# Kernel tuning notes

Hardware: AMD Instinct MI355X
Metric: run time of the kernel (lower is better)

The kernel has to match this reference:

```python
import jax, jax.numpy as jnp
import numpy as np
from jax import lax


def _lin_weights(in_size, out_size):
    # torch F.interpolate(mode='bilinear', align_corners=False) source indices
    scale = in_size / out_size
    src = (jnp.arange(out_size, dtype=jnp.float32) + 0.5) * scale - 0.5
    src = jnp.maximum(src, 0.0)
    i0 = jnp.minimum(jnp.floor(src).astype(jnp.int32), in_size - 1)
    i1 = jnp.minimum(i0 + 1, in_size - 1)
    w = src - i0.astype(jnp.float32)
    return i0, i1, w


def bilinear_resize(x, out_h, out_w):
    # x: (..., H, W) -> (..., out_h, out_w), separable bilinear
    H, W = x.shape[-2], x.shape[-1]
    i0, i1, wh = _lin_weights(H, out_h)
    j0, j1, ww = _lin_weights(W, out_w)
    x = x[..., i0, :] * (1.0 - wh)[:, None] + x[..., i1, :] * wh[:, None]
    x = x[..., :, j0] * (1.0 - ww) + x[..., :, j1] * ww
    return x


def setup_inputs() -> dict:
    key = jax.random.key(0)
    ks = jax.random.split(key, 16)
    b, H, W = 16, 56, 56
    n = H * W
    dim, heads, dh, agent_num = 512, 8, 64, 49
    ID = heads * dh  # inner_dim == dim
    s = 0.02
    return {
        'x': jax.random.normal(ks[0], (b, n, dim), jnp.float32),
        'H': H, 'W': W,
        'q_w': s * jax.random.normal(ks[1], (dim, ID), jnp.float32),
        'q_b': s * jax.random.normal(ks[2], (ID,), jnp.float32),
        'kv_w': s * jax.random.normal(ks[3], (dim, 2 * ID), jnp.float32),
        'kv_b': s * jax.random.normal(ks[4], (2 * ID,), jnp.float32),
        'proj_w': s * jax.random.normal(ks[5], (ID, dim), jnp.float32),
        'proj_b': s * jax.random.normal(ks[6], (dim,), jnp.float32),
        'dwc_w': s * jax.random.normal(ks[7], (ID, 1, 3, 3), jnp.float32),
        'dwc_b': s * jax.random.normal(ks[8], (ID,), jnp.float32),
        'an_bias': s * jax.random.normal(ks[9], (heads, agent_num, 7, 7), jnp.float32),
        'na_bias': s * jax.random.normal(ks[10], (heads, agent_num, 7, 7), jnp.float32),
        'ah_bias': s * jax.random.normal(ks[11], (1, heads, agent_num, H, 1), jnp.float32),
        'aw_bias': s * jax.random.normal(ks[12], (1, heads, agent_num, 1, W), jnp.float32),
        'ha_bias': s * jax.random.normal(ks[13], (1, heads, H, 1, agent_num), jnp.float32),
        'wa_bias': s * jax.random.normal(ks[14], (1, heads, 1, W, agent_num), jnp.float32),
    }


def reference(x, H, W, q_w, q_b, kv_w, kv_b, proj_w, proj_b, dwc_w, dwc_b,
              an_bias, na_bias, ah_bias, aw_bias, ha_bias, wa_bias):
    b, n, c = x.shape
    heads, agent_num = an_bias.shape[0], an_bias.shape[1]
    ID = q_w.shape[1]
    dh = ID // heads
    scale = dh ** -0.5
    pool = int(round(agent_num ** 0.5))  # 7

    q = x @ q_w + q_b                      # (b, n, ID)
    kv = x @ kv_w + kv_b                   # (b, n, 2*ID)  (sr_ratio == 1)
    k, v = kv[..., :ID], kv[..., ID:]

    # adaptive avg pool of q on the (H, W) grid -> agent tokens (b, agent_num, ID)
    qi = q.reshape(b, pool, H // pool, pool, W // pool, ID)
    agent = qi.mean(axis=(2, 4)).reshape(b, agent_num, ID)

    qh = q.reshape(b, n, heads, dh).transpose(0, 2, 1, 3)          # (b,h,n,d)
    kh = k.reshape(b, n, heads, dh).transpose(0, 2, 1, 3)
    vh = v.reshape(b, n, heads, dh).transpose(0, 2, 1, 3)
    ah = agent.reshape(b, agent_num, heads, dh).transpose(0, 2, 1, 3)  # (b,h,a,d)

    # stage 1: agent tokens attend to k/v, with interpolated + factored position bias
    pb1 = bilinear_resize(an_bias, H, W).reshape(1, heads, agent_num, n)
    pb2 = (ah_bias + aw_bias).reshape(1, heads, agent_num, n)
    s1 = jnp.einsum('bhad,bhnd->bhan', ah * scale, kh) + pb1 + pb2
    agent_attn = jax.nn.softmax(s1, axis=-1)                        # (b,h,a,n)
    agent_v = jnp.einsum('bhan,bhnd->bhad', agent_attn, vh)         # (b,h,a,d)

    # stage 2: queries attend to agent tokens
    ab1 = bilinear_resize(na_bias, H, W).reshape(1, heads, agent_num, n).transpose(0, 1, 3, 2)
    ab2 = (ha_bias + wa_bias).reshape(1, heads, n, agent_num)
    s2 = jnp.einsum('bhnd,bhad->bhna', qh * scale, ah) + ab1 + ab2
    q_attn = jax.nn.softmax(s2, axis=-1)                            # (b,h,n,a)
    out = jnp.einsum('bhna,bhad->bhnd', q_attn, agent_v)
    out = out.transpose(0, 2, 1, 3).reshape(b, n, ID)

    # depthwise 3x3 conv over v as spatial residual
    v_img = v.reshape(b, H, W, ID).transpose(0, 3, 1, 2)            # (b,ID,H,W)
    dwc = lax.conv_general_dilated(v_img, dwc_w, (1, 1), 'SAME',
                                   feature_group_count=ID,
                                   dimension_numbers=('NCHW', 'OIHW', 'NCHW'))
    dwc = dwc + dwc_b[None, :, None, None]
    out = out + dwc.transpose(0, 2, 3, 1).reshape(b, n, ID)

    return out @ proj_w + proj_b
```

## Files before the change

### kernel.cpp

```cpp
#include <hip/hip_runtime.h>
#include <hip/hip_bf16.h>

#define DEV __device__ __forceinline__

typedef __attribute__((ext_vector_type(4))) float f32x4;
typedef __attribute__((ext_vector_type(8))) short bf8_t;
typedef __attribute__((ext_vector_type(4))) unsigned int u32x4;

static constexpr float QSCALE = 0.125f;

DEV float bflo(unsigned int w){ union{unsigned int i; float f;} x; x.i = w << 16; return x.f; }
DEV float bfhi(unsigned int w){ union{unsigned int i; float f;} x; x.i = w & 0xffff0000u; return x.f; }
DEV float bf2f(unsigned short u){ union{unsigned int i; float f;} x; x.i = ((unsigned int)u) << 16; return x.f; }
DEV unsigned short f2bf(float f){
  union{float f; unsigned int i;} x; x.f = f;
  unsigned int i = x.i;
  i += 0x7fffu + ((i >> 16) & 1u);
  return (unsigned short)(i >> 16);
}
DEV unsigned int pack2(float a, float b){ return (unsigned int)f2bf(a) | ((unsigned int)f2bf(b) << 16); }

DEV void mfma_acc(f32x4& c, const bf8_t& a, const bf8_t& b){
  asm volatile("v_mfma_f32_16x16x32_bf16 %0, %1, %2, %0" : "+v"(c) : "v"(a), "v"(b));
}

DEV float wred_max(float v){
  #pragma unroll
  for (int m = 1; m < 64; m <<= 1) v = fmaxf(v, __shfl_xor(v, m));
  return v;
}
DEV float wred_sum(float v){
  #pragma unroll
  for (int m = 1; m < 64; m <<= 1) v += __shfl_xor(v, m);
  return v;
}

__global__ void k_prep(const float* __restrict__ qw, const float* __restrict__ kvw,
                       const float* __restrict__ pw, const float* __restrict__ qb,
                       const float* __restrict__ kvb,
                       unsigned short* __restrict__ wqkvt, unsigned short* __restrict__ wprojt,
                       float* __restrict__ qkvbias){
  const int i0 = blockIdx.x * blockDim.x + threadIdx.x;
  const int stride = gridDim.x * blockDim.x;
  for (int idx = i0; idx < 1536*512; idx += stride){
    int n = idx >> 9, k = idx & 511;
    float v = (n < 512) ? qw[k*512 + n] : kvw[k*1024 + (n - 512)];
    wqkvt[idx] = f2bf(v);
  }
  for (int idx = i0; idx < 512*512; idx += stride){
    int n = idx >> 9, k = idx & 511;
    wprojt[idx] = f2bf(pw[k*512 + n]);
  }
  for (int idx = i0; idx < 1536; idx += stride)
    qkvbias[idx] = (idx < 512) ? qb[idx] : kvb[idx - 512];
}

__global__ void k_cvt_x(const float* __restrict__ x, unsigned short* __restrict__ xb){
  const long total8 = (long)50176*512/8;
  for (long i = (long)blockIdx.x*blockDim.x + threadIdx.x; i < total8; i += (long)gridDim.x*blockDim.x){
    const float4* p = (const float4*)(x + i*8);
    float4 a = p[0], b = p[1];
    u32x4 o;
    o.x = pack2(a.x, a.y); o.y = pack2(a.z, a.w);
    o.z = pack2(b.x, b.y); o.w = pack2(b.z, b.w);
    *(u32x4*)(xb + i*8) = o;
  }
}

template<bool OUT_BF>
__global__ __launch_bounds__(256) void k_gemm(const unsigned short* __restrict__ A,
    const unsigned short* __restrict__ Bt, const float* __restrict__ bias,
    void* __restrict__ Cp, const int N){
  __shared__ unsigned short Al[128][40];
  __shared__ unsigned short Bl[128][40];
  const int tid = threadIdx.x, lane = tid & 63, w = tid >> 6;
  const int m0 = blockIdx.y * 128, n0 = blockIdx.x * 128;
  const int wr = (w >> 1) * 64, wc = (w & 1) * 64;
  const int fr = lane & 15, kg = lane >> 4;
  f32x4 acc[4][4] = {};
  for (int kt = 0; kt < 16; ++kt){
    const int k0 = kt * 32;
    __syncthreads();
    #pragma unroll
    for (int cc = 0; cc < 2; ++cc){
      const int c = tid + cc*256;
      const int row = c >> 2, kb = c & 3;
      u32x4 va = *(const u32x4*)(A  + (size_t)(m0 + row)*512 + k0 + kb*8);
      u32x4 vb = *(const u32x4*)(Bt + (size_t)(n0 + row)*512 + k0 + kb*8);
      *(u32x4*)&Al[row][kb*8] = va;
      *(u32x4*)&Bl[row][kb*8] = vb;
    }
    __syncthreads();
    bf8_t af[4], bfm[4];
    #pragma unroll
    for (int i = 0; i < 4; ++i){
      af[i]  = *(const bf8_t*)&Al[wr + i*16 + fr][kg*8];
      bfm[i] = *(const bf8_t*)&Bl[wc + i*16 + fr][kg*8];
    }
    #pragma unroll
    for (int i = 0; i < 4; ++i)
      #pragma unroll
      for (int j = 0; j < 4; ++j)
        mfma_acc(acc[i][j], af[i], bfm[j]);
  }
  const int rb = (lane >> 4) * 4;
  #pragma unroll
  for (int j = 0; j < 4; ++j){
    const int col = n0 + wc + j*16 + fr;
    const float bs = bias[col];
    #pragma unroll
    for (int i = 0; i < 4; ++i){
      #pragma unroll
      for (int r = 0; r < 4; ++r){
        const int row = m0 + wr + i*16 + rb + r;
        float v = acc[i][j][r] + bs;
        if (OUT_BF) ((unsigned short*)Cp)[(size_t)row*N + col] = f2bf(v);
        else        ((float*)Cp)[(size_t)row*N + col] = v;
      }
    }
  }
}

__global__ void k_pool(const unsigned short* __restrict__ qkv, float* __restrict__ agent){
  const int b = blockIdx.x / 49, a = blockIdx.x % 49;
  const int p1 = a / 7, p2 = a % 7;
  for (int c = threadIdx.x; c < 512; c += 256){
    float s = 0.f;
    for (int r = 0; r < 8; ++r)
      for (int cc = 0; cc < 8; ++cc){
        int pix = (p1*8 + r)*56 + p2*8 + cc;
        s += bf2f(qkv[((size_t)b*3136 + pix)*1536 + c]);
      }
    agent[((size_t)b*49 + a)*512 + c] = s * (1.0f/64.0f);
  }
}

DEV void lin_w(int o, int& i0, int& i1, float& w){
  float src = (o + 0.5f)*0.125f - 0.5f;
  src = fmaxf(src, 0.f);
  int f = (int)floorf(src);
  i0 = min(f, 6); i1 = min(i0 + 1, 6); w = src - (float)i0;
}

__global__ void k_pb(const float* __restrict__ an, const float* __restrict__ ahb,
                     const float* __restrict__ awb, float* __restrict__ pbs){
  const int tot = 8*49*3136;
  for (int idx = blockIdx.x*blockDim.x + threadIdx.x; idx < tot; idx += gridDim.x*blockDim.x){
    int n = idx % 3136, ha = idx / 3136;
    int y = n / 56, x = n % 56;
    int iy0, iy1, ix0, ix1; float wy, wx;
    lin_w(y, iy0, iy1, wy); lin_w(x, ix0, ix1, wx);
    const float* t = an + (size_t)ha*49;
    float v0 = t[iy0*7+ix0]*(1.f-wy) + t[iy1*7+ix0]*wy;
    float v1 = t[iy0*7+ix1]*(1.f-wy) + t[iy1*7+ix1]*wy;
    float v = v0*(1.f-wx) + v1*wx;
    pbs[idx] = v + ahb[ha*56 + y] + awb[ha*56 + x];
  }
}

__global__ void k_ab(const float* __restrict__ na, const float* __restrict__ hab,
                     const float* __restrict__ wab, float* __restrict__ absumT){
  const int tot = 8*49*3136;
  for (int idx = blockIdx.x*blockDim.x + threadIdx.x; idx < tot; idx += gridDim.x*blockDim.x){
    int n = idx % 3136, ha = idx / 3136;
    int a = ha % 49, h = ha / 49;
    int y = n / 56, x = n % 56;
    int iy0, iy1, ix0, ix1; float wy, wx;
    lin_w(y, iy0, iy1, wy); lin_w(x, ix0, ix1, wx);
    const float* t = na + (size_t)ha*49;
    float v0 = t[iy0*7+ix0]*(1.f-wy) + t[iy1*7+ix0]*wy;
    float v1 = t[iy0*7+ix1]*(1.f-wy) + t[iy1*7+ix1]*wy;
    float v = v0*(1.f-wx) + v1*wx;
    absumT[idx] = v + hab[(h*56+y)*49 + a] + wab[(h*56+x)*49 + a];
  }
}

__global__ __launch_bounds__(256) void k_attn1(const unsigned short* __restrict__ qkv,
    const float* __restrict__ agent, const float* __restrict__ pbs,
    float* __restrict__ pacc, float* __restrict__ pml){
  const int bi = blockIdx.x;
  const int sp = bi % 7, h = (bi/7) & 7, b = bi / 56;
  const int tid = threadIdx.x, lane = tid & 63, w = tid >> 6;
  const int c = lane & 15, kg = lane >> 4;

  __shared__ unsigned short ag[64][72];
  __shared__ unsigned short Kl[64][72];
  __shared__ unsigned short Vt[64][72];
  __shared__ unsigned short Pl[4][16][72];

  for (int it = tid; it < 64*8; it += 256){
    int a = it >> 3, o = it & 7;
    u32x4 wv = {0,0,0,0};
    if (a < 49){
      const float* p = agent + ((size_t)b*49 + a)*512 + h*64 + o*8;
      f32x4 lo = *(const f32x4*)p, hi = *(const f32x4*)(p+4);
      wv.x = pack2(lo.x*QSCALE, lo.y*QSCALE);
      wv.y = pack2(lo.z*QSCALE, lo.w*QSCALE);
      wv.z = pack2(hi.x*QSCALE, hi.y*QSCALE);
      wv.w = pack2(hi.z*QSCALE, hi.w*QSCALE);
    }
    *(u32x4*)&ag[a][o*8] = wv;
  }
  __syncthreads();
  bf8_t agf[2];
  agf[0] = *(const bf8_t*)&ag[w*16 + c][kg*8];
  agf[1] = *(const bf8_t*)&ag[w*16 + c][kg*8 + 32];

  const int aw = w*16 + c;
  const int amin = aw < 49 ? aw : 48;
  const bool areal = aw < 49;
  const float* pbrow = pbs + ((size_t)(h*49 + amin))*3136 + sp*448;

  float m_ = -1e30f, l_ = 0.f;
  f32x4 acc[4] = {};

  for (int t = 0; t < 7; ++t){
    const int gn0 = sp*448 + t*64;
    f32x4 pb4[4];
    #pragma unroll
    for (int i = 0; i < 4; ++i)
      pb4[i] = *(const f32x4*)(pbrow + t*64 + 16*i + 4*kg);

    __syncthreads();
    #pragma unroll
    for (int ii = 0; ii < 2; ++ii){
      int it = tid + ii*256;
      int pix = it >> 3, o = it & 7;
      const unsigned short* kp = qkv + ((size_t)b*3136 + gn0 + pix)*1536 + 512 + h*64 + o*8;
      *(u32x4*)&Kl[pix][o*8] = *(const u32x4*)kp;
    }
    #pragma unroll
    for (int ii = 0; ii < 2; ++ii){
      int it = tid + ii*256;
      int pix = it & 63, o = it >> 6;
      const unsigned short* vp = qkv + ((size_t)b*3136 + gn0 + pix)*1536 + 1024 + h*64 + o*8;
      u32x4 vv = *(const u32x4*)vp;
      unsigned int vals[4] = {vv.x, vv.y, vv.z, vv.w};
      #pragma unroll
      for (int q = 0; q < 4; ++q){
        Vt[o*8 + 2*q][pix]     = (unsigned short)(vals[q] & 0xffffu);
        Vt[o*8 + 2*q + 1][pix] = (unsigned short)(vals[q] >> 16);
      }
    }
    __syncthreads();

    f32x4 sa[4] = {};
    #pragma unroll
    for (int i = 0; i < 4; ++i){
      bf8_t kf0 = *(const bf8_t*)&Kl[i*16 + c][kg*8];
      bf8_t kf1 = *(const bf8_t*)&Kl[i*16 + c][kg*8 + 32];
      mfma_acc(sa[i], kf0, agf[0]);
      mfma_acc(sa[i], kf1, agf[1]);
    }

    float s16[4][4]; float mx = -1e30f;
    #pragma unroll
    for (int i = 0; i < 4; ++i)
      #pragma unroll
      for (int r = 0; r < 4; ++r){
        float sv = areal ? (sa[i][r] + pb4[i][r]) : -1e30f;
        s16[i][r] = sv; mx = fmaxf(mx, sv);
      }
    mx = fmaxf(mx, __shfl_xor(mx, 16));
    mx = fmaxf(mx, __shfl_xor(mx, 32));
    float mn = fmaxf(m_, mx);
    float al = __expf(m_ - mn);
    float rs = 0.f;
    #pragma unroll
    for (int i = 0; i < 4; ++i)
      #pragma unroll
      for (int r = 0; r < 4; ++r){
        float p = __expf(s16[i][r] - mn);
        s16[i][r] = p; rs += p;
      }
    rs += __shfl_xor(rs, 16);
    rs += __shfl_xor(rs, 32);
    m_ = mn; l_ = l_*al + rs;

    #pragma unroll
    for (int i = 0; i < 4; ++i){
      uint2 pw;
      pw.x = pack2(s16[i][0], s16[i][1]);
      pw.y = pack2(s16[i][2], s16[i][3]);
      *(uint2*)&Pl[w][c][16*i + 4*kg] = pw;
    }

    float al_s[4];
    #pragma unroll
    for (int r = 0; r < 4; ++r) al_s[r] = __shfl(al, 4*kg + r);
    #pragma unroll
    for (int j = 0; j < 4; ++j)
      #pragma unroll
      for (int r = 0; r < 4; ++r) acc[j][r] *= al_s[r];

    bf8_t pf0 = *(const bf8_t*)&Pl[w][c][kg*8];
    bf8_t pf1 = *(const bf8_t*)&Pl[w][c][kg*8 + 32];
    #pragma unroll
    for (int j = 0; j < 4; ++j){
      bf8_t vf0 = *(const bf8_t*)&Vt[j*16 + c][kg*8];
      bf8_t vf1 = *(const bf8_t*)&Vt[j*16 + c][kg*8 + 32];
      mfma_acc(acc[j], pf0, vf0);
      mfma_acc(acc[j], pf1, vf1);
    }
  }

  const int base = ((b*8 + h)*7 + sp)*49;
  #pragma unroll
  for (int r = 0; r < 4; ++r){
    const int a = w*16 + 4*kg + r;
    if (a < 49){
      float* dst = pacc + (size_t)(base + a)*64 + c;
      #pragma unroll
      for (int j = 0; j < 4; ++j) dst[16*j] = acc[j][r];
    }
  }
  if (kg == 0 && areal){
    pml[(base + aw)*2]     = m_;
    pml[(base + aw)*2 + 1] = l_;
  }
}

__global__ void k_merge(const float* __restrict__ pacc, const float* __restrict__ pml,
                        float* __restrict__ agentv){
  const int gw = blockIdx.x*4 + (threadIdx.x >> 6);
  const int lane = threadIdx.x & 63;
  if (gw >= 16*8*49) return;
  const int a = gw % 49, bh = gw / 49;
  float ms[7], ls[7], M = -1e30f;
  #pragma unroll
  for (int s = 0; s < 7; ++s){
    int base = (bh*7 + s)*49 + a;
    ms[s] = pml[base*2]; ls[s] = pml[base*2 + 1];
    M = fmaxf(M, ms[s]);
  }
  float L = 0.f, o = 0.f;
  #pragma unroll
  for (int s = 0; s < 7; ++s){
    float e = __expf(ms[s] - M);
    L += ls[s]*e;
    o += pacc[(size_t)((bh*7 + s)*49 + a)*64 + lane]*e;
  }
  agentv[(size_t)(bh*49 + a)*64 + lane] = o / L;
}

__global__ __launch_bounds__(256) void k_attn2(const unsigned short* __restrict__ qkv,
    const float* __restrict__ agent, const float* __restrict__ agentv,
    const float* __restrict__ absumT, unsigned short* __restrict__ outb){
  const int blk = blockIdx.x;
  const int bh = blk / 13, tloc = blk % 13;
  const int b = bh >> 3, h = bh & 7;
  const int tid = threadIdx.x, lane = tid & 63, w = tid >> 6;
  const int c = lane & 15, kg = lane >> 4;

  __shared__ unsigned short ag[64][72];
  __shared__ unsigned short avT[64][72];
  __shared__ unsigned short Pl[4][16][72];

  for (int it = tid; it < 64*8; it += 256){
    int a = it >> 3, o = it & 7;
    u32x4 wv = {0,0,0,0};
    if (a < 49){
      const float* p = agent + ((size_t)b*49 + a)*512 + h*64 + o*8;
      f32x4 lo = *(const f32x4*)p, hi = *(const f32x4*)(p+4);
      wv.x = pack2(lo.x*QSCALE, lo.y*QSCALE);
      wv.y = pack2(lo.z*QSCALE, lo.w*QSCALE);
      wv.z = pack2(hi.x*QSCALE, hi.y*QSCALE);
      wv.w = pack2(hi.z*QSCALE, hi.w*QSCALE);
    }
    *(u32x4*)&ag[a][o*8] = wv;
  }
  for (int it = tid; it < 64*64; it += 256){
    int a = it >> 6, d = it & 63;
    avT[d][a] = (a < 49) ? f2bf(agentv[((size_t)bh*49 + a)*64 + d]) : (unsigned short)0;
  }
  __syncthreads();

  const int ti = tloc*4 + w;
  if (ti >= 49) return;
  const int pix0 = ti*64;

  bf8_t af[4][2];
  #pragma unroll
  for (int i = 0; i < 4; ++i){
    af[i][0] = *(const bf8_t*)&ag[i*16 + c][kg*8];
    af[i][1] = *(const bf8_t*)&ag[i*16 + c][kg*8 + 32];
  }

  for (int j = 0; j < 4; ++j){
    const int pix = pix0 + 16*j + c;
    const unsigned short* qp = qkv + ((size_t)b*3136 + pix)*1536 + h*64;
    bf8_t qf0 = *(const bf8_t*)(qp + kg*8);
    bf8_t qf1 = *(const bf8_t*)(qp + kg*8 + 32);
    f32x4 sa[4] = {};
    #pragma unroll
    for (int i = 0; i < 4; ++i){
      mfma_acc(sa[i], af[i][0], qf0);
      mfma_acc(sa[i], af[i][1], qf1);
    }
    float s16[4][4]; float mx = -1e30f;
    #pragma unroll
    for (int i = 0; i < 4; ++i){
      #pragma unroll
      for (int r = 0; r < 4; ++r){
        int a = 16*i + 4*kg + r;
        int am = a < 49 ? a : 48;
        float bias = absumT[((size_t)h*49 + am)*3136 + pix];
        float sv = (a < 49) ? (sa[i][r] + bias) : -1e30f;
        s16[i][r] = sv; mx = fmaxf(mx, sv);
      }
    }
    mx = fmaxf(mx, __shfl_xor(mx, 16));
    mx = fmaxf(mx, __shfl_xor(mx, 32));
    float rs = 0.f;
    #pragma unroll
    for (int i = 0; i < 4; ++i){
      #pragma unroll
      for (int r = 0; r < 4; ++r){
        float p = __expf(s16[i][r] - mx);
        s16[i][r] = p; rs += p;
      }
    }
    rs += __shfl_xor(rs, 16);
    rs += __shfl_xor(rs, 32);
    #pragma unroll
    for (int i = 0; i < 4; ++i){
      uint2 pw;
      pw.x = pack2(s16[i][0], s16[i][1]);
      pw.y = pack2(s16[i][2], s16[i][3]);
      *(uint2*)&Pl[w][c][16*i + 4*kg] = pw;
    }
    bf8_t pf0 = *(const bf8_t*)&Pl[w][c][kg*8];
    bf8_t pf1 = *(const bf8_t*)&Pl[w][c][kg*8 + 32];
    f32x4 acc[4] = {};
    #pragma unroll
    for (int jd = 0; jd < 4; ++jd){
      bf8_t vf0 = *(const bf8_t*)&avT[jd*16 + c][kg*8];
      bf8_t vf1 = *(const bf8_t*)&avT[jd*16 + c][kg*8 + 32];
      mfma_acc(acc[jd], pf0, vf0);
      mfma_acc(acc[jd], pf1, vf1);
    }
    float l_s[4];
    #pragma unroll
    for (int r = 0; r < 4; ++r) l_s[r] = __shfl(rs, 4*kg + r);
    #pragma unroll
    for (int r = 0; r < 4; ++r){
      const int prow = pix0 + 16*j + 4*kg + r;
      unsigned short* op = outb + ((size_t)b*3136 + prow)*512 + h*64;
      float inv = 1.0f / l_s[r];
      #pragma unroll
      for (int jd = 0; jd < 4; ++jd)
        op[jd*16 + c] = f2bf(acc[jd][r] * inv);
    }
  }
}

__global__ __launch_bounds__(256) void k_dwc(const unsigned short* __restrict__ qkv,
    const float* __restrict__ dwcw, const float* __restrict__ dwcb,
    unsigned short* __restrict__ outb){
  const int b = blockIdx.x / 56, y = blockIdx.x % 56;
  const int tid = threadIdx.x;
  const int cg = tid & 127, xh = tid >> 7;
  const int c0 = cg*4;
  float wv[9][4], bv[4];
  #pragma unroll
  for (int j = 0; j < 4; ++j){
    bv[j] = dwcb[c0 + j];
    #pragma unroll
    for (int t = 0; t < 9; ++t) wv[t][j] = dwcw[(c0 + j)*9 + t];
  }
  for (int xi = 0; xi < 28; ++xi){
    const int x = xh*28 + xi;
    float o[4] = {bv[0], bv[1], bv[2], bv[3]};
    #pragma unroll
    for (int ky = 0; ky < 3; ++ky){
      int ny = y + ky - 1;
      if (ny < 0 || ny >= 56) continue;
      #pragma unroll
      for (int kx = 0; kx < 3; ++kx){
        int nx = x + kx - 1;
        if (nx < 0 || nx >= 56) continue;
        const unsigned short* vp = qkv + ((size_t)b*3136 + ny*56 + nx)*1536 + 1024 + c0;
        unsigned int v01 = *(const unsigned int*)vp;
        unsigned int v23 = *((const unsigned int*)vp + 1);
        const int t = ky*3 + kx;
        o[0] += wv[t][0]*bflo(v01); o[1] += wv[t][1]*bfhi(v01);
        o[2] += wv[t][2]*bflo(v23); o[3] += wv[t][3]*bfhi(v23);
      }
    }
    unsigned short* op = outb + ((size_t)b*3136 + y*56 + x)*512 + c0;
    unsigned int a01 = *(unsigned int*)op;
    unsigned int a23 = *((unsigned int*)op + 1);
    o[0] += bflo(a01); o[1] += bfhi(a01);
    o[2] += bflo(a23); o[3] += bfhi(a23);
    *(unsigned int*)op       = pack2(o[0], o[1]);
    *((unsigned int*)op + 1) = pack2(o[2], o[3]);
  }
}

extern "C" void kernel_launch(void* const* d_in, const int* in_sizes, int n_in,
                              void* d_out, int out_size, void* d_ws, size_t ws_size,
                              hipStream_t stream){
  const float* x       = (const float*)d_in[0];
  const float* q_w     = (const float*)d_in[3];
  const float* q_b     = (const float*)d_in[4];
  const float* kv_w    = (const float*)d_in[5];
  const float* kv_b    = (const float*)d_in[6];
  const float* proj_w  = (const float*)d_in[7];
  const float* proj_b  = (const float*)d_in[8];
  const float* dwc_w   = (const float*)d_in[9];
  const float* dwc_b   = (const float*)d_in[10];
  const float* an_bias = (const float*)d_in[11];
  const float* na_bias = (const float*)d_in[12];
  const float* ah_bias = (const float*)d_in[13];
  const float* aw_bias = (const float*)d_in[14];
  const float* ha_bias = (const float*)d_in[15];
  const float* wa_bias = (const float*)d_in[16];

  char* ws = (char*)d_ws;
  size_t off = 0;
  auto alloc = [&](size_t bytes) -> void* {
    void* p = ws + off;
    off += (bytes + 255) & ~(size_t)255;
    return p;
  };
  unsigned short* xb     = (unsigned short*)alloc((size_t)50176*512*2);
  unsigned short* qkv    = (unsigned short*)alloc((size_t)50176*1536*2);
  unsigned short* wqkvt  = (unsigned short*)alloc((size_t)1536*512*2);
  unsigned short* wprojt = (unsigned short*)alloc((size_t)512*512*2);
  float* qkvb   = (float*)alloc((size_t)1536*4);
  float* agent  = (float*)alloc((size_t)16*49*512*4);
  float* agentv = (float*)alloc((size_t)16*8*49*64*4);
  float* pbs    = (float*)alloc((size_t)8*49*3136*4);
  float* absumT = (float*)alloc((size_t)8*49*3136*4);
  float* pacc   = (float*)alloc((size_t)16*8*8*49*64*4);
  float* pml    = (float*)alloc((size_t)16*8*8*49*2*4);
  unsigned short* outb = (unsigned short*)alloc((size_t)50176*512*2);
  if (off > ws_size) return;

  k_prep<<<512, 256, 0, stream>>>(q_w, kv_w, proj_w, q_b, kv_b, wqkvt, wprojt, qkvb);
  k_cvt_x<<<2048, 256, 0, stream>>>(x, xb);
  dim3 g1(12, 392);
  k_gemm<true><<<g1, 256, 0, stream>>>(xb, wqkvt, qkvb, qkv, 1536);
  k_pool<<<784, 256, 0, stream>>>(qkv, agent);
  k_pb<<<1024, 256, 0, stream>>>(an_bias, ah_bias, aw_bias, pbs);
  k_ab<<<1024, 256, 0, stream>>>(na_bias, ha_bias, wa_bias, absumT);
  k_attn1<<<896, 256, 0, stream>>>(qkv, agent, pbs, pacc, pml);
  k_merge<<<1568, 256, 0, stream>>>(pacc, pml, agentv);
  k_attn2<<<1664, 256, 0, stream>>>(qkv, agent, agentv, absumT, outb);
  k_dwc<<<896, 256, 0, stream>>>(qkv, dwc_w, dwc_b, outb);
  dim3 g2(4, 392);
  k_gemm<false><<<g2, 256, 0, stream>>>(outb, wprojt, proj_b, d_out, 512);
}
```

Before: 414.8 us.

## Use direct global-to-LDS loads in GEMM and remap blocks for XCD locality

The GEMM tile staging now uses global_load_lds, which writes 16 bytes per lane straight into shared memory and skips the register round trip. The LDS row padding is removed so the writes stay contiguous, which may bring back bank conflicts on the fragment reads. The grid becomes 1D with a block-index swizzle that places consecutive M-tiles on the same XCD (bid&7), aiming for better L2 reuse of the A rows and weight tiles. Both the QKV and output projection GEMMs use the new mapping.

Result: faster. 404.4 us (-2.5%).

```diff
diff --git a/kernel.cpp b/kernel.cpp
--- a/kernel.cpp
+++ b/kernel.cpp
@@ -22,6 +22,12 @@
 
 DEV void mfma_acc(f32x4& c, const bf8_t& a, const bf8_t& b){
   asm volatile("v_mfma_f32_16x16x32_bf16 %0, %1, %2, %0" : "+v"(c) : "v"(a), "v"(b));
+}
+
+DEV void cp16(unsigned short* l, const unsigned short* g){
+  __builtin_amdgcn_global_load_lds(
+      (const __attribute__((address_space(1))) unsigned int*)(const void*)g,
+      (__attribute__((address_space(3))) unsigned int*)(void*)l, 16, 0, 0);
 }
 
 DEV float wred_max(float v){
@@ -70,26 +76,35 @@
 template<bool OUT_BF>
 __global__ __launch_bounds__(256) void k_gemm(const unsigned short* __restrict__ A,
     const unsigned short* __restrict__ Bt, const float* __restrict__ bias,
-    void* __restrict__ Cp, const int N){
-  __shared__ unsigned short Al[128][40];
-  __shared__ unsigned short Bl[128][40];
+    void* __restrict__ Cp, const int N, const int nxb){
+  __shared__ unsigned short Al[128][32];
+  __shared__ unsigned short Bl[128][32];
   const int tid = threadIdx.x, lane = tid & 63, w = tid >> 6;
-  const int m0 = blockIdx.y * 128, n0 = blockIdx.x * 128;
+  const int bid = blockIdx.x;
+  const int cxd = bid & 7, kk = bid >> 3;
+  const int yi = kk / nxb, xb = kk - yi*nxb;
+  const int m0 = (cxd + 8*yi) * 128, n0 = xb * 128;
   const int wr = (w >> 1) * 64, wc = (w & 1) * 64;
   const int fr = lane & 15, kg = lane >> 4;
+  const int srow = lane >> 2, sp = lane & 3;
+
+  const unsigned short* gA0 = A  + (size_t)(m0 + w*32 + srow)*512 + sp*8;
+  const unsigned short* gA1 = gA0 + (size_t)16*512;
+  const unsigned short* gB0 = Bt + (size_t)(n0 + w*32 + srow)*512 + sp*8;
+  const unsigned short* gB1 = gB0 + (size_t)16*512;
+  unsigned short* lA0 = &Al[w*32][0];
+  unsigned short* lA1 = &Al[w*32 + 16][0];
+  unsigned short* lB0 = &Bl[w*32][0];
+  unsigned short* lB1 = &Bl[w*32 + 16][0];
+
   f32x4 acc[4][4] = {};
   for (int kt = 0; kt < 16; ++kt){
     const int k0 = kt * 32;
     __syncthreads();
-    #pragma unroll
-    for (int cc = 0; cc < 2; ++cc){
-      const int c = tid + cc*256;
-      const int row = c >> 2, kb = c & 3;
-      u32x4 va = *(const u32x4*)(A  + (size_t)(m0 + row)*512 + k0 + kb*8);
-      u32x4 vb = *(const u32x4*)(Bt + (size_t)(n0 + row)*512 + k0 + kb*8);
-      *(u32x4*)&Al[row][kb*8] = va;
-      *(u32x4*)&Bl[row][kb*8] = vb;
-    }
+    cp16(lA0, gA0 + k0);
+    cp16(lA1, gA1 + k0);
+    cp16(lB0, gB0 + k0);
+    cp16(lB1, gB1 + k0);
     __syncthreads();
     bf8_t af[4], bfm[4];
     #pragma unroll
@@ -539,8 +554,7 @@
 
   k_prep<<<512, 256, 0, stream>>>(q_w, kv_w, proj_w, q_b, kv_b, wqkvt, wprojt, qkvb);
   k_cvt_x<<<2048, 256, 0, stream>>>(x, xb);
-  dim3 g1(12, 392);
-  k_gemm<true><<<g1, 256, 0, stream>>>(xb, wqkvt, qkvb, qkv, 1536);
+  k_gemm<true><<<4704, 256, 0, stream>>>(xb, wqkvt, qkvb, qkv, 1536, 12);
   k_pool<<<784, 256, 0, stream>>>(qkv, agent);
   k_pb<<<1024, 256, 0, stream>>>(an_bias, ah_bias, aw_bias, pbs);
   k_ab<<<1024, 256, 0, stream>>>(na_bias, ha_bias, wa_bias, absumT);
@@ -548,6 +562,5 @@
   k_merge<<<1568, 256, 0, stream>>>(pacc, pml, agentv);
   k_attn2<<<1664, 256, 0, stream>>>(qkv, agent, agentv, absumT, outb);
   k_dwc<<<896, 256, 0, stream>>>(qkv, dwc_w, dwc_b, outb);
-  dim3 g2(4, 392);
-  k_gemm<false><<<g2, 256, 0, stream>>>(outb, wprojt, proj_b, d_out, 512);
-}
+  k_gemm<false><<<1568, 256, 0, stream>>>(outb, wprojt, proj_b, d_out, 512, 4);
+}
```

## Rewrite GEMM with 256x256 tiles, direct global-to-LDS double buffering

Applied to the files above, without the earlier changes.

Replaces the 128x128 register-staged GEMM with a 512-thread, 256x256-tile kernel. Tiles are loaded straight into LDS with global_load_lds, double-buffered so the next K slice loads while MFMAs run on the current one. It also adds an XCD-aware block remap and raises wave priority around the MFMA block. The goals are more reuse per tile, hidden load latency and fewer register round trips, at the cost of more registers per wave and unpadded LDS rows that may cause bank conflicts.

Result: slower. 452.8 us (+9.2%).

```diff
diff --git a/kernel.cpp b/kernel.cpp
--- a/kernel.cpp
+++ b/kernel.cpp
@@ -23,6 +23,16 @@
 DEV void mfma_acc(f32x4& c, const bf8_t& a, const bf8_t& b){
   asm volatile("v_mfma_f32_16x16x32_bf16 %0, %1, %2, %0" : "+v"(c) : "v"(a), "v"(b));
 }
+
+DEV void cp16(unsigned short* l, const unsigned short* g){
+  __builtin_amdgcn_global_load_lds(
+      (const __attribute__((address_space(1))) unsigned int*)(const void*)g,
+      (__attribute__((address_space(3))) unsigned int*)(void*)l, 16, 0, 0);
+}
+
+#define FENCE asm volatile("" ::: "memory")
+#define SBAR  do{ FENCE; __builtin_amdgcn_s_barrier(); FENCE; __builtin_amdgcn_sched_barrier(0); }while(0)
+#define WAIT_VM(n) do{ asm volatile("s_waitcnt vmcnt(" #n ")" ::: "memory"); __builtin_amdgcn_sched_barrier(0); }while(0)
 
 DEV float wred_max(float v){
   #pragma unroll
@@ -68,52 +78,77 @@
 }
 
 template<bool OUT_BF>
-__global__ __launch_bounds__(256) void k_gemm(const unsigned short* __restrict__ A,
+__global__ __launch_bounds__(512) void k_gemm2(const unsigned short* __restrict__ A,
     const unsigned short* __restrict__ Bt, const float* __restrict__ bias,
-    void* __restrict__ Cp, const int N){
-  __shared__ unsigned short Al[128][40];
-  __shared__ unsigned short Bl[128][40];
+    void* __restrict__ Cp, const int N, const int nN){
+  __shared__ unsigned short Al[2][256][32];
+  __shared__ unsigned short Bl[2][256][32];
   const int tid = threadIdx.x, lane = tid & 63, w = tid >> 6;
-  const int m0 = blockIdx.y * 128, n0 = blockIdx.x * 128;
-  const int wr = (w >> 1) * 64, wc = (w & 1) * 64;
-  const int fr = lane & 15, kg = lane >> 4;
-  f32x4 acc[4][4] = {};
+  const int wgid = (blockIdx.x & 7) * (gridDim.x >> 3) + (blockIdx.x >> 3);
+  const int mi = wgid / nN, ni = wgid % nN;
+  const int m0 = mi*256, n0 = ni*256;
+  const int wr = w >> 2, wc = w & 3;
+  const int c = lane & 15, kg = lane >> 4;
+  const int srow = lane >> 2, sslot = lane & 3;
+
+  const unsigned short* gA = A  + (size_t)(m0 + w*16 + srow)*512 + sslot*8;
+  const unsigned short* gB = Bt + (size_t)(n0 + w*16 + srow)*512 + sslot*8;
+
+  f32x4 acc[8][4] = {};
+
+  #define STAGE(kt) do{ \
+    const int _b = (kt) & 1; const int _k0 = (kt)*32; \
+    cp16(&Al[_b][w*16][0],       gA + _k0); \
+    cp16(&Al[_b][128 + w*16][0], gA + (size_t)128*512 + _k0); \
+    cp16(&Bl[_b][w*16][0],       gB + _k0); \
+    cp16(&Bl[_b][128 + w*16][0], gB + (size_t)128*512 + _k0); \
+  }while(0)
+
+  STAGE(0); STAGE(1);
+  WAIT_VM(4);
+  SBAR;
+
+  #pragma unroll 2
   for (int kt = 0; kt < 16; ++kt){
-    const int k0 = kt * 32;
-    __syncthreads();
-    #pragma unroll
-    for (int cc = 0; cc < 2; ++cc){
-      const int c = tid + cc*256;
-      const int row = c >> 2, kb = c & 3;
-      u32x4 va = *(const u32x4*)(A  + (size_t)(m0 + row)*512 + k0 + kb*8);
-      u32x4 vb = *(const u32x4*)(Bt + (size_t)(n0 + row)*512 + k0 + kb*8);
-      *(u32x4*)&Al[row][kb*8] = va;
-      *(u32x4*)&Bl[row][kb*8] = vb;
-    }
-    __syncthreads();
-    bf8_t af[4], bfm[4];
-    #pragma unroll
-    for (int i = 0; i < 4; ++i){
-      af[i]  = *(const bf8_t*)&Al[wr + i*16 + fr][kg*8];
-      bfm[i] = *(const bf8_t*)&Bl[wc + i*16 + fr][kg*8];
-    }
-    #pragma unroll
-    for (int i = 0; i < 4; ++i)
-      #pragma unroll
-      for (int j = 0; j < 4; ++j)
-        mfma_acc(acc[i][j], af[i], bfm[j]);
-  }
-  const int rb = (lane >> 4) * 4;
-  #pragma unroll
-  for (int j = 0; j < 4; ++j){
-    const int col = n0 + wc + j*16 + fr;
+    const int buf = kt & 1;
+    bf8_t b4[4], a8[8];
+    #pragma unroll
+    for (int nf = 0; nf < 4; ++nf)
+      b4[nf] = *(const bf8_t*)&Bl[buf][wc*64 + nf*16 + c][kg*8];
+    #pragma unroll
+    for (int mf = 0; mf < 8; ++mf)
+      a8[mf] = *(const bf8_t*)&Al[buf][wr*128 + mf*16 + c][kg*8];
+    __builtin_amdgcn_s_setprio(1);
+    #pragma unroll
+    for (int mf = 0; mf < 8; ++mf)
+      #pragma unroll
+      for (int nf = 0; nf < 4; ++nf)
+        mfma_acc(acc[mf][nf], a8[mf], b4[nf]);
+    __builtin_amdgcn_s_setprio(0);
+
+    if (kt == 15) break;
+    SBAR;
+    if (kt < 14){
+      STAGE(kt+2);
+      WAIT_VM(4);
+    } else {
+      WAIT_VM(0);
+    }
+    SBAR;
+  }
+  #undef STAGE
+
+  const int rb = kg*4;
+  #pragma unroll
+  for (int nf = 0; nf < 4; ++nf){
+    const int col = n0 + wc*64 + nf*16 + c;
     const float bs = bias[col];
     #pragma unroll
-    for (int i = 0; i < 4; ++i){
+    for (int mf = 0; mf < 8; ++mf){
       #pragma unroll
       for (int r = 0; r < 4; ++r){
-        const int row = m0 + wr + i*16 + rb + r;
-        float v = acc[i][j][r] + bs;
+        const int row = m0 + wr*128 + mf*16 + rb + r;
+        float v = acc[mf][nf][r] + bs;
         if (OUT_BF) ((unsigned short*)Cp)[(size_t)row*N + col] = f2bf(v);
         else        ((float*)Cp)[(size_t)row*N + col] = v;
       }
@@ -539,8 +574,7 @@
 
   k_prep<<<512, 256, 0, stream>>>(q_w, kv_w, proj_w, q_b, kv_b, wqkvt, wprojt, qkvb);
   k_cvt_x<<<2048, 256, 0, stream>>>(x, xb);
-  dim3 g1(12, 392);
-  k_gemm<true><<<g1, 256, 0, stream>>>(xb, wqkvt, qkvb, qkv, 1536);
+  k_gemm2<true><<<1176, 512, 0, stream>>>(xb, wqkvt, qkvb, qkv, 1536, 6);
   k_pool<<<784, 256, 0, stream>>>(qkv, agent);
   k_pb<<<1024, 256, 0, stream>>>(an_bias, ah_bias, aw_bias, pbs);
   k_ab<<<1024, 256, 0, stream>>>(na_bias, ha_bias, wa_bias, absumT);
@@ -548,6 +582,5 @@
   k_merge<<<1568, 256, 0, stream>>>(pacc, pml, agentv);
   k_attn2<<<1664, 256, 0, stream>>>(qkv, agent, agentv, absumT, outb);
   k_dwc<<<896, 256, 0, stream>>>(qkv, dwc_w, dwc_b, outb);
-  dim3 g2(4, 392);
-  k_gemm<false><<<g2, 256, 0, stream>>>(outb, wprojt, proj_b, d_out, 512);
-}
+  k_gemm2<false><<<392, 512, 0, stream>>>(outb, wprojt, proj_b, d_out, 512, 2);
+}
```
